# Optimization experiments

Measured on AMD Instinct MI355X. Metric: run time of the kernel, lower is better.

## Reference

```python
import jax, jax.numpy as jnp
import numpy as np
from jax import lax

EPS = 1e-5

def conv2d(x, w, b, pad):
    # x: [N,C,H,W], w: [O,I,kh,kw]
    y = lax.conv_general_dilated(x, w, (1, 1), [(pad, pad), (pad, pad)],
                                 dimension_numbers=('NCHW', 'OIHW', 'NCHW'))
    return y + b[None, :, None, None]

def bn(x, g, b, axes, pshape):
    # training-mode batch norm (biased variance), matching torch BatchNorm2d in train()
    m = jnp.mean(x, axes, keepdims=True)
    v = jnp.var(x, axes, keepdims=True)
    return (x - m) * lax.rsqrt(v + EPS) * g.reshape(pshape) + b.reshape(pshape)

def maxpool2(x):
    return lax.reduce_window(x, -jnp.inf, lax.max, (1, 1, 2, 2), (1, 1, 2, 2), 'VALID')

def setup_inputs() -> dict:
    key = jax.random.key(0)
    ks = jax.random.split(key, 8)
    B, S, C, H, W = 8, 20, 16, 96, 96
    inp = {
        'anchor': jax.random.normal(ks[0], (B, C, H, W), jnp.float32),
        'support': jax.random.normal(ks[1], (B, S, C, H, W), jnp.float32),
        'cw': jax.random.normal(ks[2], (16, 16, 3, 3), jnp.float32) * 0.1,
        'cb': jnp.zeros((16,), jnp.float32),
        'cg': jnp.ones((16,), jnp.float32),
        'cbt': jnp.zeros((16,), jnp.float32),
        'pw': jax.random.normal(ks[3], (16, 32, 1, 1), jnp.float32) * 0.1,
        'pb': jnp.zeros((16,), jnp.float32),
        'pg': jnp.ones((16,), jnp.float32),
        'pbt': jnp.zeros((16,), jnp.float32),
        'jw': jax.random.normal(ks[4], (16, 16, 3, 3), jnp.float32) * 0.1,
        'jb': jnp.zeros((16,), jnp.float32),
        'jg': jnp.ones((16,), jnp.float32),
        'jbt': jnp.zeros((16,), jnp.float32),
        'rw': jax.random.normal(ks[5], (16, 16, 3, 3), jnp.float32) * 0.1,
        'rb': jnp.zeros((16,), jnp.float32),
        'rg': jnp.ones((16,), jnp.float32),
        'rbt': jnp.zeros((16,), jnp.float32),
    }
    return inp

def reference(anchor, support, cw, cb, cg, cbt, pw, pb, pg, pbt,
              jw, jb, jg, jbt, rw, rb, rg, rbt):
    B, S, C, H, W = support.shape
    # reshaper(anchor): conv3x3 -> BN -> ReLU -> maxpool2   (BN stats over B,H,W)
    ax = maxpool2(jax.nn.relu(bn(conv2d(anchor, rw, rb, 1), rg, rbt, (0, 2, 3), (1, -1, 1, 1))))
    # reshaper(support flattened): BN stats pooled over B*S,H,W (matches torch view(-1,...))
    sflat = support.reshape(B * S, C, H, W)
    sr = maxpool2(jax.nn.relu(bn(conv2d(sflat, rw, rb, 1), rg, rbt, (0, 2, 3), (1, -1, 1, 1))))
    sr = sr.reshape(B, S, C, H // 2, W // 2)
    # concentrator(support flattened)
    sx = jax.nn.relu(bn(conv2d(sflat, cw, cb, 1), cg, cbt, (0, 2, 3), (1, -1, 1, 1)))
    sx = sx.reshape(B, S, C, H, W)
    # leave-one-out sum via total-sum trick (O(S) instead of O(S^2))
    loo = sx.sum(axis=1, keepdims=True) - sx              # [B,S,C,H,W]
    cat = jnp.concatenate([support, loo], axis=2)         # [B,S,2C,H,W]
    pe = conv2d(cat.reshape(B * S, 2 * C, H, W), pw, pb, 0).reshape(B, S, C, H, W)
    # torch loop applies perm_equi per-i: BN stats over (B,H,W) for each support index
    pe = jax.nn.relu(bn(pe, pg, pbt, (0, 3, 4), (1, 1, -1, 1, 1)))
    deep = pe.mean(axis=1)                                # [B,C,H,W]
    # projector: conv3x3 -> BN -> softmax over channels -> maxpool2
    proj = maxpool2(jax.nn.softmax(bn(conv2d(deep, jw, jb, 1), jg, jbt, (0, 2, 3), (1, -1, 1, 1)), axis=1))
    anchor_out = ax * proj                                # [B,C,H/2,W/2]
    support_out = sr * proj[:, None]                      # [B,S,C,H/2,W/2]
    return anchor_out, support_out
```

## Files before the change

### kernel.cpp

```cpp
#include <hip/hip_runtime.h>
#include <stdint.h>

#define EPS_BN 1e-5f

typedef __attribute__((ext_vector_type(8))) short short8;
typedef __attribute__((ext_vector_type(4))) float floatx4;

__device__ __forceinline__ unsigned short f2bf(float f) {
    unsigned u = __builtin_bit_cast(unsigned, f);
    u += 0x7fffu + ((u >> 16) & 1u);
    return (unsigned short)(u >> 16);
}
__device__ __forceinline__ float bf2f(unsigned short h) {
    unsigned u = ((unsigned)h) << 16;
    return __builtin_bit_cast(float, u);
}
__device__ __forceinline__ void unpack8(uint4 q, float* v) {
    v[0] = bf2f((unsigned short)q.x); v[1] = bf2f((unsigned short)(q.x >> 16));
    v[2] = bf2f((unsigned short)q.y); v[3] = bf2f((unsigned short)(q.y >> 16));
    v[4] = bf2f((unsigned short)q.z); v[5] = bf2f((unsigned short)(q.z >> 16));
    v[6] = bf2f((unsigned short)q.w); v[7] = bf2f((unsigned short)(q.w >> 16));
}
__device__ __forceinline__ uint4 pack8(const float* v) {
    uint4 q;
    q.x = (unsigned)f2bf(v[0]) | ((unsigned)f2bf(v[1]) << 16);
    q.y = (unsigned)f2bf(v[2]) | ((unsigned)f2bf(v[3]) << 16);
    q.z = (unsigned)f2bf(v[4]) | ((unsigned)f2bf(v[5]) << 16);
    q.w = (unsigned)f2bf(v[6]) | ((unsigned)f2bf(v[7]) << 16);
    return q;
}

__device__ __forceinline__ void async_copy16(const unsigned short* g, unsigned short* l) {
    __builtin_amdgcn_global_load_lds(
        (const __attribute__((address_space(1))) unsigned int*)(const void*)g,
        (__attribute__((address_space(3))) unsigned int*)(void*)l,
        16, 0, 0);
}

__device__ __forceinline__ void bn_coef(const float* st, int n, int c, float invN,
                                        const float* gg, const float* bb,
                                        float* scl, float* shf) {
    const float mean = st[c] * invN;
    const float var = st[n + c] * invN - mean * mean;
    const float sc = gg[c & 15] * rsqrtf(var + EPS_BN);
    scl[c] = sc;
    shf[c] = bb[c & 15] - mean * sc;
}

__global__ __launch_bounds__(256)
void pack_kernel(const float* __restrict__ support, const float* __restrict__ anchor,
                 unsigned short* __restrict__ spad, unsigned short* __restrict__ apad)
{
    const int idx = blockIdx.x * 256 + threadIdx.x;
    if (idx >= 168 * 9604) return;
    const int img = idx / 9604;
    const int rem = idx - img * 9604;
    const int pr = rem / 98, pc = rem - pr * 98;
    const int gh = pr - 1, gw = pc - 1;
    const bool ok = (gh >= 0) & (gh < 96) & (gw >= 0) & (gw < 96);
    const float* src = (img < 160) ? (support + (size_t)img * 147456)
                                   : (anchor + (size_t)(img - 160) * 147456);
    unsigned short* dst = (img < 160) ? (spad + (size_t)img * 9604 * 16)
                                      : (apad + (size_t)(img - 160) * 9604 * 16);
    const int gbase = gh * 96 + gw;
    unsigned pk[8];
    #pragma unroll
    for (int c = 0; c < 8; ++c) {
        const float v0 = ok ? src[(2 * c) * 9216 + gbase] : 0.f;
        const float v1 = ok ? src[(2 * c + 1) * 9216 + gbase] : 0.f;
        pk[c] = (unsigned)f2bf(v0) | ((unsigned)f2bf(v1) << 16);
    }
    const int sw = (pc >> 2) & 1;
    unsigned short* p = dst + (size_t)rem * 16;
    *(uint4*)(p + (sw << 3)) = make_uint4(pk[0], pk[1], pk[2], pk[3]);
    *(uint4*)(p + ((sw ^ 1) << 3)) = make_uint4(pk[4], pk[5], pk[6], pk[7]);
}

__global__ void packw_kernel(const float* __restrict__ rw, const float* __restrict__ cw,
                             const float* __restrict__ jw, unsigned short* __restrict__ frag,
                             float* __restrict__ stats)
{
    const int tid = threadIdx.x;
    if (blockIdx.x == 4) {
        #pragma unroll
        for (int k = 0; k < 3; ++k) stats[k * 256 + tid] = 0.f;
        return;
    }
    const int idx = blockIdx.x * 256 + tid;
    if (idx >= 960) return;
    const int combo = idx >> 6, lane = idx & 63;
    const int cv = combo / 5, j = combo - cv * 5;
    const float* w = (cv == 0) ? rw : (cv == 1) ? cw : jw;
    const int o = lane & 15, g = lane >> 4;
    unsigned short e8[8];
    #pragma unroll
    for (int e = 0; e < 8; ++e) {
        const int k = j * 32 + g * 8 + e;
        unsigned short val = 0;
        if (k < 144) {
            const int t = k >> 4, i = k & 15;
            const int kh = t / 3, kw = t - kh * 3;
            val = f2bf(w[((o * 16 + i) * 3 + kh) * 3 + kw]);
        }
        e8[e] = val;
    }
    *(uint4*)(frag + ((size_t)combo * 64 + lane) * 8) =
        make_uint4((unsigned)e8[0] | ((unsigned)e8[1] << 16), (unsigned)e8[2] | ((unsigned)e8[3] << 16),
                   (unsigned)e8[4] | ((unsigned)e8[5] << 16), (unsigned)e8[6] | ((unsigned)e8[7] << 16));
}

template<bool TWO, bool POOLA>
__global__ __launch_bounds__(256)
void conv3x3_kernel(const unsigned short* __restrict__ in,
                    const unsigned short* __restrict__ fragA, const float* __restrict__ bA,
                    const unsigned short* __restrict__ fragB, const float* __restrict__ bB,
                    unsigned short* __restrict__ outA, unsigned short* __restrict__ outB,
                    float* __restrict__ statsA, float* __restrict__ statsB)
{
    __shared__ __align__(16) unsigned short lds[10 * 98 * 16];
    __shared__ float red[4][4][16];

    const int tid = threadIdx.x;
    const int lane = tid & 63;
    const int wv = tid >> 6;
    const int img = blockIdx.x / 12;
    const int r0b = blockIdx.x - img * 12;

    const unsigned short* gsrc = in + ((size_t)img * 9604 + r0b * 8 * 98) * 16;
    #pragma unroll
    for (int k = 0; k < 8; ++k) {
        const int chunk = k * 256 + tid;
        if (chunk < 1960)
            async_copy16(gsrc + (size_t)chunk * 8, lds + (k * 256 + wv * 64) * 8);
    }

    const int n = lane & 15, g = lane >> 4;
    short8 fA[5], fB[5];
    #pragma unroll
    for (int j = 0; j < 5; ++j) {
        fA[j] = *(const short8*)(fragA + ((size_t)j * 64 + lane) * 8);
        if (TWO) fB[j] = *(const short8*)(fragB + ((size_t)j * 64 + lane) * 8);
    }
    const float4 bA4 = *(const float4*)(bA + 4 * g);
    float4 bB4 = make_float4(0.f, 0.f, 0.f, 0.f);
    if (TWO) bB4 = *(const float4*)(bB + 4 * g);
    const float biasA[4] = {bA4.x, bA4.y, bA4.z, bA4.w};
    const float biasB[4] = {bB4.x, bB4.y, bB4.z, bB4.w};

    __syncthreads();

    float s1A[4] = {0.f, 0.f, 0.f, 0.f}, s2A[4] = {0.f, 0.f, 0.f, 0.f};
    float s1B[4] = {0.f, 0.f, 0.f, 0.f}, s2B[4] = {0.f, 0.f, 0.f, 0.f};

    for (int cg = 0; cg < 6; ++cg) {
        float pA[2][4], pB[2][4];
        #pragma unroll
        for (int tr = 0; tr < 2; ++tr) {
            const int lr = 2 * wv + tr;
            floatx4 aA = {0.f, 0.f, 0.f, 0.f};
            floatx4 aB = {0.f, 0.f, 0.f, 0.f};
            #pragma unroll
            for (int j = 0; j < 5; ++j) {
                const int t = (j < 4) ? (2 * j + (g >> 1)) : 8;
                const int kh = t / 3, kw = t - kh * 3;
                const int ldscol = cg * 16 + n + kw;
                const int half = (g & 1) ^ ((ldscol >> 2) & 1);
                const short8 a = *(const short8*)&lds[((lr + kh) * 98 + ldscol) * 16 + (half << 3)];
                aA = __builtin_amdgcn_mfma_f32_16x16x32_bf16(fA[j], a, aA, 0, 0, 0);
                if (TWO) aB = __builtin_amdgcn_mfma_f32_16x16x32_bf16(fB[j], a, aB, 0, 0, 0);
            }
            #pragma unroll
            for (int r = 0; r < 4; ++r) {
                const float vA = aA[r] + biasA[r];
                pA[tr][r] = vA; s1A[r] += vA; s2A[r] += vA * vA;
                if (TWO) {
                    const float vB = aB[r] + biasB[r];
                    pB[tr][r] = vB; s1B[r] += vB; s2B[r] += vB * vB;
                }
            }
            const int grow = r0b * 8 + lr;
            const size_t pixbase = ((size_t)img * 9216 + grow * 96 + cg * 16 + n) * 16 + 4 * g;
            if (TWO)
                *(uint2*)(outB + pixbase) =
                    make_uint2((unsigned)f2bf(pB[tr][0]) | ((unsigned)f2bf(pB[tr][1]) << 16),
                               (unsigned)f2bf(pB[tr][2]) | ((unsigned)f2bf(pB[tr][3]) << 16));
            if (!POOLA)
                *(uint2*)(outA + pixbase) =
                    make_uint2((unsigned)f2bf(pA[tr][0]) | ((unsigned)f2bf(pA[tr][1]) << 16),
                               (unsigned)f2bf(pA[tr][2]) | ((unsigned)f2bf(pA[tr][3]) << 16));
        }
        if (POOLA) {
            float pm[4];
            #pragma unroll
            for (int r = 0; r < 4; ++r) {
                pm[r] = fmaxf(pA[0][r], pA[1][r]);
                pm[r] = fmaxf(pm[r], __shfl_xor(pm[r], 1));
            }
            if (!(n & 1)) {
                const int orow = r0b * 4 + wv;
                const size_t ob = ((size_t)img * 2304 + orow * 48 + cg * 8 + (n >> 1)) * 16 + 4 * g;
                *(uint2*)(outA + ob) =
                    make_uint2((unsigned)f2bf(pm[0]) | ((unsigned)f2bf(pm[1]) << 16),
                               (unsigned)f2bf(pm[2]) | ((unsigned)f2bf(pm[3]) << 16));
            }
        }
    }

    #pragma unroll
    for (int r = 0; r < 4; ++r) {
        #pragma unroll
        for (int d = 1; d < 16; d <<= 1) {
            s1A[r] += __shfl_xor(s1A[r], d); s2A[r] += __shfl_xor(s2A[r], d);
            if (TWO) { s1B[r] += __shfl_xor(s1B[r], d); s2B[r] += __shfl_xor(s2B[r], d); }
        }
    }
    if (n == 0) {
        #pragma unroll
        for (int r = 0; r < 4; ++r) {
            red[wv][0][g * 4 + r] = s1A[r]; red[wv][1][g * 4 + r] = s2A[r];
            if (TWO) { red[wv][2][g * 4 + r] = s1B[r]; red[wv][3][g * 4 + r] = s2B[r]; }
        }
    }
    __syncthreads();
    if (tid < (TWO ? 64 : 32)) {
        const int st = tid >> 4, oc = tid & 15;
        const float v = red[0][st][oc] + red[1][st][oc] + red[2][st][oc] + red[3][st][oc];
        float* dst = (st < 2) ? statsA : statsB;
        atomicAdd(&dst[(st & 1) * 16 + oc], v);
    }
}

__global__ __launch_bounds__(256)
void sxsum_kernel(const unsigned short* __restrict__ sx, const float* __restrict__ statsSx,
                  const float* __restrict__ cgm, const float* __restrict__ cbt,
                  float* __restrict__ out, unsigned short* __restrict__ deeppad)
{
    __shared__ float scl[16], shf[16];
    __shared__ float part[128][17];
    const int tid = threadIdx.x;
    if (blockIdx.x < 13) {
        const int idx = blockIdx.x * 256 + tid;
        if (idx < 8 * 388) {
            const int img = idx / 388;
            const int h = idx - img * 388;
            int pr, pc;
            if (h < 98)       { pr = 0;           pc = h; }
            else if (h < 196) { pr = 97;          pc = h - 98; }
            else if (h < 292) { pr = h - 196 + 1; pc = 0; }
            else              { pr = h - 292 + 1; pc = 97; }
            unsigned short* p = deeppad + ((size_t)img * 9604 + pr * 98 + pc) * 16;
            *(uint4*)p = make_uint4(0, 0, 0, 0);
            *(uint4*)(p + 8) = make_uint4(0, 0, 0, 0);
        }
    }
    if (tid < 16) bn_coef(statsSx, 16, tid, 1.f / 1474560.f, cgm, cbt, scl, shf);
    const int b = blockIdx.x / 72;
    const int chunk = blockIdx.x - b * 72;
    const int px = tid & 127, sg = tid >> 7;
    const int pix = chunk * 128 + px;
    __syncthreads();
    float acc[16];
    #pragma unroll
    for (int c = 0; c < 16; ++c) acc[c] = 0.f;
    const unsigned short* p = sx + ((size_t)((b * 20) + sg * 10) * 9216 + pix) * 16;
    for (int s = 0; s < 10; ++s) {
        float v[16];
        unpack8(*(const uint4*)p, v);
        unpack8(*(const uint4*)(p + 8), v + 8);
        #pragma unroll
        for (int c = 0; c < 16; ++c) acc[c] += fmaxf(v[c] * scl[c] + shf[c], 0.f);
        p += 9216 * 16;
    }
    if (sg == 1) {
        #pragma unroll
        for (int c = 0; c < 16; ++c) part[px][c] = acc[c];
    }
    __syncthreads();
    if (sg == 0) {
        #pragma unroll
        for (int c = 0; c < 16; ++c) acc[c] += part[px][c];
        float* o = out + ((size_t)b * 9216 + pix) * 16;
        #pragma unroll
        for (int q = 0; q < 4; ++q)
            *(float4*)(o + 4 * q) = make_float4(acc[4 * q], acc[4 * q + 1], acc[4 * q + 2], acc[4 * q + 3]);
    }
}

__global__ __launch_bounds__(256)
void pe_kernel(const unsigned short* __restrict__ spad, unsigned short* __restrict__ sxpe,
               const float* __restrict__ sxsum, const float* __restrict__ statsSx,
               const float* __restrict__ cgm, const float* __restrict__ cbt,
               const float* __restrict__ pw, const float* __restrict__ pb,
               float* __restrict__ statsPe)
{
    __shared__ float sscl[16], sshf[16];
    __shared__ float red[4][2][16];
    const int tid = threadIdx.x;
    if (tid < 16) bn_coef(statsSx, 16, tid, 1.f / 1474560.f, cgm, cbt, sscl, sshf);
    const int lane = tid & 63, wv = tid >> 6;
    const int p = lane & 15, g = lane >> 4;
    const int img = blockIdx.x / 9;
    const int chunk = blockIdx.x - img * 9;
    const int b = img / 20, s = img - b * 20;
    const int c0 = (g & 1) * 8;

    short8 fw;
    {
        const float4 wa = *(const float4*)(pw + p * 32 + g * 8);
        const float4 wb = *(const float4*)(pw + p * 32 + g * 8 + 4);
        fw[0] = (short)f2bf(wa.x); fw[1] = (short)f2bf(wa.y);
        fw[2] = (short)f2bf(wa.z); fw[3] = (short)f2bf(wa.w);
        fw[4] = (short)f2bf(wb.x); fw[5] = (short)f2bf(wb.y);
        fw[6] = (short)f2bf(wb.z); fw[7] = (short)f2bf(wb.w);
    }
    const float4 b4 = *(const float4*)(pb + 4 * g);
    const float bias[4] = {b4.x, b4.y, b4.z, b4.w};
    __syncthreads();
    float scl[8], shf[8];
    #pragma unroll
    for (int e = 0; e < 8; ++e) { scl[e] = sscl[c0 + e]; shf[e] = sshf[c0 + e]; }

    const unsigned short* imgspad = spad + (size_t)img * 9604 * 16;
    unsigned short* imgsx = sxpe + (size_t)img * 9216 * 16;
    const float* bsum = sxsum + (size_t)b * 9216 * 16;

    float s1[4] = {0.f, 0.f, 0.f, 0.f}, s2[4] = {0.f, 0.f, 0.f, 0.f};

    for (int it = 0; it < 16; ++it) {
        const int pix = chunk * 1024 + it * 64 + wv * 16 + p;
        short8 bf;
        if (g < 2) {
            const int row = pix / 96, col = pix - row * 96;
            const int sw = ((col + 1) >> 2) & 1;
            bf = *(const short8*)(imgspad + ((row + 1) * 98 + col + 1) * 16 + (((g ^ sw) & 1) << 3));
        } else {
            float xv[8];
            unpack8(*(const uint4*)(imgsx + (size_t)pix * 16 + c0), xv);
            const float* sm = bsum + (size_t)pix * 16 + c0;
            const float4 sma = *(const float4*)sm;
            const float4 smb = *(const float4*)(sm + 4);
            const float smv[8] = {sma.x, sma.y, sma.z, sma.w, smb.x, smb.y, smb.z, smb.w};
            #pragma unroll
            for (int e = 0; e < 8; ++e) {
                const float loo = smv[e] - fmaxf(xv[e] * scl[e] + shf[e], 0.f);
                bf[e] = (short)f2bf(loo);
            }
        }
        floatx4 acc = {0.f, 0.f, 0.f, 0.f};
        acc = __builtin_amdgcn_mfma_f32_16x16x32_bf16(fw, bf, acc, 0, 0, 0);
        const float v0 = acc[0] + bias[0], v1 = acc[1] + bias[1];
        const float v2 = acc[2] + bias[2], v3 = acc[3] + bias[3];
        s1[0] += v0; s1[1] += v1; s1[2] += v2; s1[3] += v3;
        s2[0] += v0 * v0; s2[1] += v1 * v1; s2[2] += v2 * v2; s2[3] += v3 * v3;
        *(uint2*)(imgsx + (size_t)pix * 16 + 4 * g) =
            make_uint2((unsigned)f2bf(v0) | ((unsigned)f2bf(v1) << 16),
                       (unsigned)f2bf(v2) | ((unsigned)f2bf(v3) << 16));
    }

    #pragma unroll
    for (int r = 0; r < 4; ++r) {
        #pragma unroll
        for (int d = 1; d < 16; d <<= 1) {
            s1[r] += __shfl_xor(s1[r], d);
            s2[r] += __shfl_xor(s2[r], d);
        }
    }
    if (p == 0) {
        #pragma unroll
        for (int r = 0; r < 4; ++r) { red[wv][0][g * 4 + r] = s1[r]; red[wv][1][g * 4 + r] = s2[r]; }
    }
    __syncthreads();
    if (tid < 32) {
        const int st = tid >> 4, c = tid & 15;
        const float v = red[0][st][c] + red[1][st][c] + red[2][st][c] + red[3][st][c];
        atomicAdd(&statsPe[st * 320 + s * 16 + c], v);
    }
}

__global__ __launch_bounds__(256)
void deep_kernel(const unsigned short* __restrict__ pe, const float* __restrict__ statsPe,
                 const float* __restrict__ pg, const float* __restrict__ pbt,
                 unsigned short* __restrict__ deeppad)
{
    __shared__ float scl[320], shf[320];
    __shared__ float part[128][17];
    const int tid = threadIdx.x;
    for (int i = tid; i < 320; i += 256)
        bn_coef(statsPe, 320, i, 1.f / 73728.f, pg, pbt, scl, shf);
    const int b = blockIdx.x / 72;
    const int chunk = blockIdx.x - b * 72;
    const int px = tid & 127, sg = tid >> 7;
    const int pix = chunk * 128 + px;
    __syncthreads();
    float acc[16];
    #pragma unroll
    for (int c = 0; c < 16; ++c) acc[c] = 0.f;
    const unsigned short* p = pe + ((size_t)((b * 20) + sg * 10) * 9216 + pix) * 16;
    for (int s = 0; s < 10; ++s) {
        const int si = sg * 10 + s;
        float v[16];
        unpack8(*(const uint4*)p, v);
        unpack8(*(const uint4*)(p + 8), v + 8);
        #pragma unroll
        for (int c = 0; c < 16; ++c) acc[c] += fmaxf(v[c] * scl[si * 16 + c] + shf[si * 16 + c], 0.f);
        p += 9216 * 16;
    }
    if (sg == 1) {
        #pragma unroll
        for (int c = 0; c < 16; ++c) part[px][c] = acc[c];
    }
    __syncthreads();
    if (sg == 0) {
        #pragma unroll
        for (int c = 0; c < 16; ++c) acc[c] = (acc[c] + part[px][c]) * 0.05f;
        const int row = pix / 96, col = pix - row * 96;
        const int sw = ((col + 1) >> 2) & 1;
        unsigned short* d = deeppad + ((size_t)b * 9604 + (row + 1) * 98 + col + 1) * 16;
        *(uint4*)(d + (sw << 3)) = pack8(acc);
        *(uint4*)(d + ((sw ^ 1) << 3)) = pack8(acc + 8);
    }
}

__global__ __launch_bounds__(256)
void proj_kernel(const unsigned short* __restrict__ pj, const float* __restrict__ statsJ,
                 const float* __restrict__ jg, const float* __restrict__ jbt,
                 float* __restrict__ proj)
{
    __shared__ float scl[16], shf[16];
    const int tid = threadIdx.x;
    if (tid < 16) bn_coef(statsJ, 16, tid, 1.f / 73728.f, jg, jbt, scl, shf);
    const int b = blockIdx.x / 9;
    const int opix = (blockIdx.x - b * 9) * 256 + tid;
    __syncthreads();
    const int oi = opix / 48, oj = opix - oi * 48;
    float mx[16];
    #pragma unroll
    for (int c = 0; c < 16; ++c) mx[c] = 0.f;
    #pragma unroll
    for (int dy = 0; dy < 2; ++dy) {
        const unsigned short* q = pj + ((size_t)b * 9216 + (2 * oi + dy) * 96 + 2 * oj) * 16;
        #pragma unroll
        for (int dx = 0; dx < 2; ++dx) {
            float v[16]; float mval = -1e30f;
            unpack8(*(const uint4*)(q + dx * 16), v);
            unpack8(*(const uint4*)(q + dx * 16 + 8), v + 8);
            #pragma unroll
            for (int c = 0; c < 16; ++c) { v[c] = v[c] * scl[c] + shf[c]; mval = fmaxf(mval, v[c]); }
            float ssum = 0.f;
            #pragma unroll
            for (int c = 0; c < 16; ++c) { v[c] = __expf(v[c] - mval); ssum += v[c]; }
            const float inv = 1.f / ssum;
            #pragma unroll
            for (int c = 0; c < 16; ++c) mx[c] = fmaxf(mx[c], v[c] * inv);
        }
    }
    float* o = proj + ((size_t)b * 2304 + opix) * 16;
    #pragma unroll
    for (int q2 = 0; q2 < 4; ++q2)
        *(float4*)(o + 4 * q2) = make_float4(mx[4 * q2], mx[4 * q2 + 1], mx[4 * q2 + 2], mx[4 * q2 + 3]);
}

__global__ __launch_bounds__(256)
void out_anchor_kernel(const unsigned short* __restrict__ axp, const float* __restrict__ statsAx,
                       const float* __restrict__ rg, const float* __restrict__ rbt,
                       const float* __restrict__ proj, float* __restrict__ out)
{
    __shared__ float scl[16], shf[16];
    const int tid = threadIdx.x;
    if (tid < 16) bn_coef(statsAx, 16, tid, 1.f / 73728.f, rg, rbt, scl, shf);
    const int b = blockIdx.x / 9;
    const int opix = (blockIdx.x - b * 9) * 256 + tid;
    __syncthreads();
    const unsigned short* p = axp + ((size_t)b * 2304 + opix) * 16;
    float v[16];
    unpack8(*(const uint4*)p, v);
    unpack8(*(const uint4*)(p + 8), v + 8);
    const float* pr = proj + ((size_t)b * 2304 + opix) * 16;
    #pragma unroll
    for (int c = 0; c < 16; ++c)
        out[((size_t)b * 16 + c) * 2304 + opix] = fmaxf(v[c] * scl[c] + shf[c], 0.f) * pr[c];
}

__global__ __launch_bounds__(256)
void out_support_kernel(const unsigned short* __restrict__ srp, const float* __restrict__ statsSr,
                        const float* __restrict__ rg, const float* __restrict__ rbt,
                        const float* __restrict__ proj, float* __restrict__ out)
{
    __shared__ float scl[16], shf[16];
    const int tid = threadIdx.x;
    if (tid < 16) bn_coef(statsSr, 16, tid, 1.f / 1474560.f, rg, rbt, scl, shf);
    const int bs = blockIdx.x / 9;
    const int opix = (blockIdx.x - bs * 9) * 256 + tid;
    const int b = bs / 20;
    __syncthreads();
    const unsigned short* p = srp + ((size_t)bs * 2304 + opix) * 16;
    float v[16];
    unpack8(*(const uint4*)p, v);
    unpack8(*(const uint4*)(p + 8), v + 8);
    const float* pr = proj + ((size_t)b * 2304 + opix) * 16;
    #pragma unroll
    for (int c = 0; c < 16; ++c)
        out[((size_t)bs * 16 + c) * 2304 + opix] = fmaxf(v[c] * scl[c] + shf[c], 0.f) * pr[c];
}

extern "C" void kernel_launch(void* const* d_in, const int* in_sizes, int n_in,
                              void* d_out, int out_size, void* d_ws, size_t ws_size,
                              hipStream_t stream)
{
    const float* anchor  = (const float*)d_in[0];
    const float* support = (const float*)d_in[1];
    const float* cw  = (const float*)d_in[2];
    const float* cb  = (const float*)d_in[3];
    const float* cgm = (const float*)d_in[4];
    const float* cbt = (const float*)d_in[5];
    const float* pw  = (const float*)d_in[6];
    const float* pb  = (const float*)d_in[7];
    const float* pg  = (const float*)d_in[8];
    const float* pbt = (const float*)d_in[9];
    const float* jw  = (const float*)d_in[10];
    const float* jb  = (const float*)d_in[11];
    const float* jg  = (const float*)d_in[12];
    const float* jbt = (const float*)d_in[13];
    const float* rw  = (const float*)d_in[14];
    const float* rb  = (const float*)d_in[15];
    const float* rg  = (const float*)d_in[16];
    const float* rbt = (const float*)d_in[17];
    float* out = (float*)d_out;

    char* ws = (char*)d_ws;
    unsigned short* spad    = (unsigned short*)ws;
    unsigned short* pre_j   = (unsigned short*)(ws + 2458624);
    float*          proj    = (float*)(ws + 4817920);
    unsigned short* apad    = (unsigned short*)(ws + 49172480);
    unsigned short* deeppad = apad;
    unsigned short* sxpe    = (unsigned short*)(ws + 51631104);
    unsigned short* srp     = (unsigned short*)(ws + 98817024);
    unsigned short* axp     = (unsigned short*)(ws + 110613504);
    float*          sxsum   = (float*)(ws + 111203328);
    unsigned short* frag    = (unsigned short*)(ws + 115921920);
    float*          stats   = (float*)(ws + 115937280);

    unsigned short* fragR = frag;
    unsigned short* fragC = frag + 5 * 64 * 8;
    unsigned short* fragJ = frag + 10 * 64 * 8;
    float* statsAx = stats,      *statsSr = stats + 32, *statsSx = stats + 64;
    float* statsPe = stats + 96, *statsJ  = stats + 736;

    pack_kernel<<<6303, 256, 0, stream>>>(support, anchor, spad, apad);
    packw_kernel<<<5, 256, 0, stream>>>(rw, cw, jw, frag, stats);

    conv3x3_kernel<true, true><<<1920, 256, 0, stream>>>(
        spad, fragR, rb, fragC, cb, srp, sxpe, statsSr, statsSx);
    conv3x3_kernel<false, true><<<96, 256, 0, stream>>>(
        apad, fragR, rb, nullptr, nullptr, axp, nullptr, statsAx, nullptr);
    sxsum_kernel<<<576, 256, 0, stream>>>(sxpe, statsSx, cgm, cbt, sxsum, deeppad);
    pe_kernel<<<1440, 256, 0, stream>>>(spad, sxpe, sxsum, statsSx, cgm, cbt, pw, pb, statsPe);
    deep_kernel<<<576, 256, 0, stream>>>(sxpe, statsPe, pg, pbt, deeppad);
    conv3x3_kernel<false, false><<<96, 256, 0, stream>>>(
        deeppad, fragJ, jb, nullptr, nullptr, pre_j, nullptr, statsJ, nullptr);
    proj_kernel<<<72, 256, 0, stream>>>(pre_j, statsJ, jg, jbt, proj);
    out_anchor_kernel<<<72, 256, 0, stream>>>(axp, statsAx, rg, rbt, proj, out);
    out_support_kernel<<<1440, 256, 0, stream>>>(srp, statsSr, rg, rbt, proj, out + 294912);
}
```

Baseline: 153.1 us.

## Merge small kernels into combined launches and split S-reduction across four groups

Folds weight packing and stats zeroing into the input pack kernel, merges the support and anchor conv launches into one grid, and merges the two output kernels into one. This cuts launch count and lets the small anchor work run alongside the support work instead of as separate, under-occupied launches. The sxsum and deep reductions now use four support groups of 5 over 64-pixel chunks, giving twice as many blocks for more parallelism. The conv kernel now takes a runtime 'two' flag instead of a template parameter, which may add divergence or register pressure.

Result: faster. 144.8 us (-5.5%).

```diff
diff --git a/kernel.cpp b/kernel.cpp
--- a/kernel.cpp
+++ b/kernel.cpp
@@ -49,9 +49,43 @@
 
 __global__ __launch_bounds__(256)
 void pack_kernel(const float* __restrict__ support, const float* __restrict__ anchor,
-                 unsigned short* __restrict__ spad, unsigned short* __restrict__ apad)
-{
-    const int idx = blockIdx.x * 256 + threadIdx.x;
+                 unsigned short* __restrict__ spad, unsigned short* __restrict__ apad,
+                 const float* __restrict__ rw, const float* __restrict__ cw,
+                 const float* __restrict__ jw, unsigned short* __restrict__ frag,
+                 float* __restrict__ stats)
+{
+    const int tid = threadIdx.x;
+    if (blockIdx.x >= 6303) {
+        const int bx = blockIdx.x - 6303;
+        if (bx == 4) {
+            #pragma unroll
+            for (int k = 0; k < 3; ++k) stats[k * 256 + tid] = 0.f;
+            return;
+        }
+        const int idx = bx * 256 + tid;
+        if (idx >= 960) return;
+        const int combo = idx >> 6, lane = idx & 63;
+        const int cv = combo / 5, j = combo - cv * 5;
+        const float* w = (cv == 0) ? rw : (cv == 1) ? cw : jw;
+        const int o = lane & 15, g = lane >> 4;
+        unsigned short e8[8];
+        #pragma unroll
+        for (int e = 0; e < 8; ++e) {
+            const int k = j * 32 + g * 8 + e;
+            unsigned short val = 0;
+            if (k < 144) {
+                const int t = k >> 4, i = k & 15;
+                const int kh = t / 3, kw = t - kh * 3;
+                val = f2bf(w[((o * 16 + i) * 3 + kh) * 3 + kw]);
+            }
+            e8[e] = val;
+        }
+        *(uint4*)(frag + ((size_t)combo * 64 + lane) * 8) =
+            make_uint4((unsigned)e8[0] | ((unsigned)e8[1] << 16), (unsigned)e8[2] | ((unsigned)e8[3] << 16),
+                       (unsigned)e8[4] | ((unsigned)e8[5] << 16), (unsigned)e8[6] | ((unsigned)e8[7] << 16));
+        return;
+    }
+    const int idx = blockIdx.x * 256 + tid;
     if (idx >= 168 * 9604) return;
     const int img = idx / 9604;
     const int rem = idx - img * 9604;
@@ -76,57 +110,21 @@
     *(uint4*)(p + ((sw ^ 1) << 3)) = make_uint4(pk[4], pk[5], pk[6], pk[7]);
 }
 
-__global__ void packw_kernel(const float* __restrict__ rw, const float* __restrict__ cw,
-                             const float* __restrict__ jw, unsigned short* __restrict__ frag,
-                             float* __restrict__ stats)
-{
-    const int tid = threadIdx.x;
-    if (blockIdx.x == 4) {
-        #pragma unroll
-        for (int k = 0; k < 3; ++k) stats[k * 256 + tid] = 0.f;
-        return;
-    }
-    const int idx = blockIdx.x * 256 + tid;
-    if (idx >= 960) return;
-    const int combo = idx >> 6, lane = idx & 63;
-    const int cv = combo / 5, j = combo - cv * 5;
-    const float* w = (cv == 0) ? rw : (cv == 1) ? cw : jw;
-    const int o = lane & 15, g = lane >> 4;
-    unsigned short e8[8];
-    #pragma unroll
-    for (int e = 0; e < 8; ++e) {
-        const int k = j * 32 + g * 8 + e;
-        unsigned short val = 0;
-        if (k < 144) {
-            const int t = k >> 4, i = k & 15;
-            const int kh = t / 3, kw = t - kh * 3;
-            val = f2bf(w[((o * 16 + i) * 3 + kh) * 3 + kw]);
-        }
-        e8[e] = val;
-    }
-    *(uint4*)(frag + ((size_t)combo * 64 + lane) * 8) =
-        make_uint4((unsigned)e8[0] | ((unsigned)e8[1] << 16), (unsigned)e8[2] | ((unsigned)e8[3] << 16),
-                   (unsigned)e8[4] | ((unsigned)e8[5] << 16), (unsigned)e8[6] | ((unsigned)e8[7] << 16));
-}
-
-template<bool TWO, bool POOLA>
-__global__ __launch_bounds__(256)
-void conv3x3_kernel(const unsigned short* __restrict__ in,
-                    const unsigned short* __restrict__ fragA, const float* __restrict__ bA,
-                    const unsigned short* __restrict__ fragB, const float* __restrict__ bB,
-                    unsigned short* __restrict__ outA, unsigned short* __restrict__ outB,
-                    float* __restrict__ statsA, float* __restrict__ statsB)
-{
-    __shared__ __align__(16) unsigned short lds[10 * 98 * 16];
-    __shared__ float red[4][4][16];
-
+template<bool POOLA>
+__device__ __forceinline__ void conv_tile(
+    unsigned short* lds, float* red,
+    const unsigned short* __restrict__ imgin,
+    const unsigned short* __restrict__ fragA, const float* __restrict__ bA,
+    const unsigned short* __restrict__ fragB, const float* __restrict__ bB,
+    unsigned short* __restrict__ outAimg, unsigned short* __restrict__ outBimg,
+    float* __restrict__ statsA, float* __restrict__ statsB,
+    const int r0b, const bool two)
+{
     const int tid = threadIdx.x;
     const int lane = tid & 63;
     const int wv = tid >> 6;
-    const int img = blockIdx.x / 12;
-    const int r0b = blockIdx.x - img * 12;
-
-    const unsigned short* gsrc = in + ((size_t)img * 9604 + r0b * 8 * 98) * 16;
+
+    const unsigned short* gsrc = imgin + (size_t)(r0b * 8 * 98) * 16;
     #pragma unroll
     for (int k = 0; k < 8; ++k) {
         const int chunk = k * 256 + tid;
@@ -139,11 +137,11 @@
     #pragma unroll
     for (int j = 0; j < 5; ++j) {
         fA[j] = *(const short8*)(fragA + ((size_t)j * 64 + lane) * 8);
-        if (TWO) fB[j] = *(const short8*)(fragB + ((size_t)j * 64 + lane) * 8);
+        if (two) fB[j] = *(const short8*)(fragB + ((size_t)j * 64 + lane) * 8);
     }
     const float4 bA4 = *(const float4*)(bA + 4 * g);
     float4 bB4 = make_float4(0.f, 0.f, 0.f, 0.f);
-    if (TWO) bB4 = *(const float4*)(bB + 4 * g);
+    if (two) bB4 = *(const float4*)(bB + 4 * g);
     const float biasA[4] = {bA4.x, bA4.y, bA4.z, bA4.w};
     const float biasB[4] = {bB4.x, bB4.y, bB4.z, bB4.w};
 
@@ -167,25 +165,25 @@
                 const int half = (g & 1) ^ ((ldscol >> 2) & 1);
                 const short8 a = *(const short8*)&lds[((lr + kh) * 98 + ldscol) * 16 + (half << 3)];
                 aA = __builtin_amdgcn_mfma_f32_16x16x32_bf16(fA[j], a, aA, 0, 0, 0);
-                if (TWO) aB = __builtin_amdgcn_mfma_f32_16x16x32_bf16(fB[j], a, aB, 0, 0, 0);
+                if (two) aB = __builtin_amdgcn_mfma_f32_16x16x32_bf16(fB[j], a, aB, 0, 0, 0);
             }
             #pragma unroll
             for (int r = 0; r < 4; ++r) {
                 const float vA = aA[r] + biasA[r];
                 pA[tr][r] = vA; s1A[r] += vA; s2A[r] += vA * vA;
-                if (TWO) {
+                if (two) {
                     const float vB = aB[r] + biasB[r];
                     pB[tr][r] = vB; s1B[r] += vB; s2B[r] += vB * vB;
                 }
             }
             const int grow = r0b * 8 + lr;
-            const size_t pixbase = ((size_t)img * 9216 + grow * 96 + cg * 16 + n) * 16 + 4 * g;
-            if (TWO)
-                *(uint2*)(outB + pixbase) =
+            const size_t pixbase = ((size_t)(grow * 96 + cg * 16 + n)) * 16 + 4 * g;
+            if (two)
+                *(uint2*)(outBimg + pixbase) =
                     make_uint2((unsigned)f2bf(pB[tr][0]) | ((unsigned)f2bf(pB[tr][1]) << 16),
                                (unsigned)f2bf(pB[tr][2]) | ((unsigned)f2bf(pB[tr][3]) << 16));
             if (!POOLA)
-                *(uint2*)(outA + pixbase) =
+                *(uint2*)(outAimg + pixbase) =
                     make_uint2((unsigned)f2bf(pA[tr][0]) | ((unsigned)f2bf(pA[tr][1]) << 16),
                                (unsigned)f2bf(pA[tr][2]) | ((unsigned)f2bf(pA[tr][3]) << 16));
         }
@@ -198,8 +196,8 @@
             }
             if (!(n & 1)) {
                 const int orow = r0b * 4 + wv;
-                const size_t ob = ((size_t)img * 2304 + orow * 48 + cg * 8 + (n >> 1)) * 16 + 4 * g;
-                *(uint2*)(outA + ob) =
+                const size_t ob = ((size_t)(orow * 48 + cg * 8 + (n >> 1))) * 16 + 4 * g;
+                *(uint2*)(outAimg + ob) =
                     make_uint2((unsigned)f2bf(pm[0]) | ((unsigned)f2bf(pm[1]) << 16),
                                (unsigned)f2bf(pm[2]) | ((unsigned)f2bf(pm[3]) << 16));
             }
@@ -211,23 +209,63 @@
         #pragma unroll
         for (int d = 1; d < 16; d <<= 1) {
             s1A[r] += __shfl_xor(s1A[r], d); s2A[r] += __shfl_xor(s2A[r], d);
-            if (TWO) { s1B[r] += __shfl_xor(s1B[r], d); s2B[r] += __shfl_xor(s2B[r], d); }
+            if (two) { s1B[r] += __shfl_xor(s1B[r], d); s2B[r] += __shfl_xor(s2B[r], d); }
         }
     }
     if (n == 0) {
         #pragma unroll
         for (int r = 0; r < 4; ++r) {
-            red[wv][0][g * 4 + r] = s1A[r]; red[wv][1][g * 4 + r] = s2A[r];
-            if (TWO) { red[wv][2][g * 4 + r] = s1B[r]; red[wv][3][g * 4 + r] = s2B[r]; }
-        }
-    }
-    __syncthreads();
-    if (tid < (TWO ? 64 : 32)) {
+            red[(wv * 4 + 0) * 16 + g * 4 + r] = s1A[r];
+            red[(wv * 4 + 1) * 16 + g * 4 + r] = s2A[r];
+            if (two) {
+                red[(wv * 4 + 2) * 16 + g * 4 + r] = s1B[r];
+                red[(wv * 4 + 3) * 16 + g * 4 + r] = s2B[r];
+            }
+        }
+    }
+    __syncthreads();
+    if (tid < (two ? 64 : 32)) {
         const int st = tid >> 4, oc = tid & 15;
-        const float v = red[0][st][oc] + red[1][st][oc] + red[2][st][oc] + red[3][st][oc];
+        const float v = red[(0 * 4 + st) * 16 + oc] + red[(1 * 4 + st) * 16 + oc] +
+                        red[(2 * 4 + st) * 16 + oc] + red[(3 * 4 + st) * 16 + oc];
         float* dst = (st < 2) ? statsA : statsB;
         atomicAdd(&dst[(st & 1) * 16 + oc], v);
     }
+}
+
+__global__ __launch_bounds__(256)
+void conv_main_kernel(const unsigned short* __restrict__ spad, const unsigned short* __restrict__ apad,
+                      const unsigned short* __restrict__ fragR, const float* __restrict__ rb,
+                      const unsigned short* __restrict__ fragC, const float* __restrict__ cb,
+                      unsigned short* __restrict__ srp, unsigned short* __restrict__ sxpe,
+                      unsigned short* __restrict__ axp,
+                      float* __restrict__ statsSr, float* __restrict__ statsSx,
+                      float* __restrict__ statsAx)
+{
+    __shared__ __align__(16) unsigned short lds[10 * 98 * 16];
+    __shared__ float red[4 * 4 * 16];
+    const bool two = blockIdx.x < 1920;
+    const int bid = two ? blockIdx.x : blockIdx.x - 1920;
+    const int img = bid / 12;
+    const int r0b = bid - img * 12;
+    const unsigned short* in = (two ? spad : apad) + (size_t)img * 9604 * 16;
+    unsigned short* outA = (two ? srp : axp) + (size_t)img * 2304 * 16;
+    unsigned short* outB = sxpe + (size_t)img * 9216 * 16;
+    conv_tile<true>(lds, red, in, fragR, rb, fragC, cb, outA, outB,
+                    two ? statsSr : statsAx, statsSx, r0b, two);
+}
+
+__global__ __launch_bounds__(256)
+void conv_j_kernel(const unsigned short* __restrict__ deeppad,
+                   const unsigned short* __restrict__ fragJ, const float* __restrict__ jb,
+                   unsigned short* __restrict__ pre_j, float* __restrict__ statsJ)
+{
+    __shared__ __align__(16) unsigned short lds[10 * 98 * 16];
+    __shared__ float red[4 * 4 * 16];
+    const int img = blockIdx.x / 12;
+    const int r0b = blockIdx.x - img * 12;
+    conv_tile<false>(lds, red, deeppad + (size_t)img * 9604 * 16, fragJ, jb, nullptr, nullptr,
+                     pre_j + (size_t)img * 9216 * 16, nullptr, statsJ, nullptr, r0b, false);
 }
 
 __global__ __launch_bounds__(256)
@@ -236,7 +274,7 @@
                   float* __restrict__ out, unsigned short* __restrict__ deeppad)
 {
     __shared__ float scl[16], shf[16];
-    __shared__ float part[128][17];
+    __shared__ float part[3][64][17];
     const int tid = threadIdx.x;
     if (blockIdx.x < 13) {
         const int idx = blockIdx.x * 256 + tid;
@@ -254,16 +292,17 @@
         }
     }
     if (tid < 16) bn_coef(statsSx, 16, tid, 1.f / 1474560.f, cgm, cbt, scl, shf);
-    const int b = blockIdx.x / 72;
-    const int chunk = blockIdx.x - b * 72;
-    const int px = tid & 127, sg = tid >> 7;
-    const int pix = chunk * 128 + px;
+    const int b = blockIdx.x / 144;
+    const int chunk = blockIdx.x - b * 144;
+    const int px = tid & 63, sg = tid >> 6;
+    const int pix = chunk * 64 + px;
     __syncthreads();
     float acc[16];
     #pragma unroll
     for (int c = 0; c < 16; ++c) acc[c] = 0.f;
-    const unsigned short* p = sx + ((size_t)((b * 20) + sg * 10) * 9216 + pix) * 16;
-    for (int s = 0; s < 10; ++s) {
+    const unsigned short* p = sx + ((size_t)(b * 20 + sg * 5) * 9216 + pix) * 16;
+    #pragma unroll
+    for (int s = 0; s < 5; ++s) {
         float v[16];
         unpack8(*(const uint4*)p, v);
         unpack8(*(const uint4*)(p + 8), v + 8);
@@ -271,14 +310,14 @@
         for (int c = 0; c < 16; ++c) acc[c] += fmaxf(v[c] * scl[c] + shf[c], 0.f);
         p += 9216 * 16;
     }
-    if (sg == 1) {
-        #pragma unroll
-        for (int c = 0; c < 16; ++c) part[px][c] = acc[c];
+    if (sg > 0) {
+        #pragma unroll
+        for (int c = 0; c < 16; ++c) part[sg - 1][px][c] = acc[c];
     }
     __syncthreads();
     if (sg == 0) {
         #pragma unroll
-        for (int c = 0; c < 16; ++c) acc[c] += part[px][c];
+        for (int c = 0; c < 16; ++c) acc[c] += part[0][px][c] + part[1][px][c] + part[2][px][c];
         float* o = out + ((size_t)b * 9216 + pix) * 16;
         #pragma unroll
         for (int q = 0; q < 4; ++q)
@@ -383,21 +422,22 @@
                  unsigned short* __restrict__ deeppad)
 {
     __shared__ float scl[320], shf[320];
-    __shared__ float part[128][17];
+    __shared__ float part[3][64][17];
     const int tid = threadIdx.x;
     for (int i = tid; i < 320; i += 256)
         bn_coef(statsPe, 320, i, 1.f / 73728.f, pg, pbt, scl, shf);
-    const int b = blockIdx.x / 72;
-    const int chunk = blockIdx.x - b * 72;
-    const int px = tid & 127, sg = tid >> 7;
-    const int pix = chunk * 128 + px;
+    const int b = blockIdx.x / 144;
+    const int chunk = blockIdx.x - b * 144;
+    const int px = tid & 63, sg = tid >> 6;
+    const int pix = chunk * 64 + px;
     __syncthreads();
     float acc[16];
     #pragma unroll
     for (int c = 0; c < 16; ++c) acc[c] = 0.f;
-    const unsigned short* p = pe + ((size_t)((b * 20) + sg * 10) * 9216 + pix) * 16;
-    for (int s = 0; s < 10; ++s) {
-        const int si = sg * 10 + s;
+    const unsigned short* p = pe + ((size_t)(b * 20 + sg * 5) * 9216 + pix) * 16;
+    #pragma unroll
+    for (int s = 0; s < 5; ++s) {
+        const int si = sg * 5 + s;
         float v[16];
         unpack8(*(const uint4*)p, v);
         unpack8(*(const uint4*)(p + 8), v + 8);
@@ -405,14 +445,15 @@
         for (int c = 0; c < 16; ++c) acc[c] += fmaxf(v[c] * scl[si * 16 + c] + shf[si * 16 + c], 0.f);
         p += 9216 * 16;
     }
-    if (sg == 1) {
-        #pragma unroll
-        for (int c = 0; c < 16; ++c) part[px][c] = acc[c];
+    if (sg > 0) {
+        #pragma unroll
+        for (int c = 0; c < 16; ++c) part[sg - 1][px][c] = acc[c];
     }
     __syncthreads();
     if (sg == 0) {
         #pragma unroll
-        for (int c = 0; c < 16; ++c) acc[c] = (acc[c] + part[px][c]) * 0.05f;
+        for (int c = 0; c < 16; ++c)
+            acc[c] = (acc[c] + part[0][px][c] + part[1][px][c] + part[2][px][c]) * 0.05f;
         const int row = pix / 96, col = pix - row * 96;
         const int sw = ((col + 1) >> 2) & 1;
         unsigned short* d = deeppad + ((size_t)b * 9604 + (row + 1) * 98 + col + 1) * 16;
@@ -461,46 +502,33 @@
 }
 
 __global__ __launch_bounds__(256)
-void out_anchor_kernel(const unsigned short* __restrict__ axp, const float* __restrict__ statsAx,
-                       const float* __restrict__ rg, const float* __restrict__ rbt,
-                       const float* __restrict__ proj, float* __restrict__ out)
+void out_kernel(const unsigned short* __restrict__ srp, const unsigned short* __restrict__ axp,
+                const float* __restrict__ statsSr, const float* __restrict__ statsAx,
+                const float* __restrict__ rg, const float* __restrict__ rbt,
+                const float* __restrict__ proj, float* __restrict__ outS,
+                float* __restrict__ outA)
 {
     __shared__ float scl[16], shf[16];
     const int tid = threadIdx.x;
-    if (tid < 16) bn_coef(statsAx, 16, tid, 1.f / 73728.f, rg, rbt, scl, shf);
-    const int b = blockIdx.x / 9;
-    const int opix = (blockIdx.x - b * 9) * 256 + tid;
-    __syncthreads();
-    const unsigned short* p = axp + ((size_t)b * 2304 + opix) * 16;
+    const bool sup = blockIdx.x < 1440;
+    if (tid < 16) {
+        if (sup) bn_coef(statsSr, 16, tid, 1.f / 1474560.f, rg, rbt, scl, shf);
+        else     bn_coef(statsAx, 16, tid, 1.f / 73728.f, rg, rbt, scl, shf);
+    }
+    const int bid = sup ? blockIdx.x : blockIdx.x - 1440;
+    const int bs = bid / 9;
+    const int opix = (bid - bs * 9) * 256 + tid;
+    const int b = sup ? bs / 20 : bs;
+    __syncthreads();
+    const unsigned short* p = (sup ? srp : axp) + ((size_t)bs * 2304 + opix) * 16;
     float v[16];
     unpack8(*(const uint4*)p, v);
     unpack8(*(const uint4*)(p + 8), v + 8);
     const float* pr = proj + ((size_t)b * 2304 + opix) * 16;
+    float* o = sup ? outS : outA;
     #pragma unroll
     for (int c = 0; c < 16; ++c)
-        out[((size_t)b * 16 + c) * 2304 + opix] = fmaxf(v[c] * scl[c] + shf[c], 0.f) * pr[c];
-}
-
-__global__ __launch_bounds__(256)
-void out_support_kernel(const unsigned short* __restrict__ srp, const float* __restrict__ statsSr,
-                        const float* __restrict__ rg, const float* __restrict__ rbt,
-                        const float* __restrict__ proj, float* __restrict__ out)
-{
-    __shared__ float scl[16], shf[16];
-    const int tid = threadIdx.x;
-    if (tid < 16) bn_coef(statsSr, 16, tid, 1.f / 1474560.f, rg, rbt, scl, shf);
-    const int bs = blockIdx.x / 9;
-    const int opix = (blockIdx.x - bs * 9) * 256 + tid;
-    const int b = bs / 20;
-    __syncthreads();
-    const unsigned short* p = srp + ((size_t)bs * 2304 + opix) * 16;
-    float v[16];
-    unpack8(*(const uint4*)p, v);
-    unpack8(*(const uint4*)(p + 8), v + 8);
-    const float* pr = proj + ((size_t)b * 2304 + opix) * 16;
-    #pragma unroll
-    for (int c = 0; c < 16; ++c)
-        out[((size_t)bs * 16 + c) * 2304 + opix] = fmaxf(v[c] * scl[c] + shf[c], 0.f) * pr[c];
+        o[((size_t)bs * 16 + c) * 2304 + opix] = fmaxf(v[c] * scl[c] + shf[c], 0.f) * pr[c];
 }
 
 extern "C" void kernel_launch(void* const* d_in, const int* in_sizes, int n_in,
@@ -546,19 +574,14 @@
     float* statsAx = stats,      *statsSr = stats + 32, *statsSx = stats + 64;
     float* statsPe = stats + 96, *statsJ  = stats + 736;
 
-    pack_kernel<<<6303, 256, 0, stream>>>(support, anchor, spad, apad);
-    packw_kernel<<<5, 256, 0, stream>>>(rw, cw, jw, frag, stats);
-
-    conv3x3_kernel<true, true><<<1920, 256, 0, stream>>>(
-        spad, fragR, rb, fragC, cb, srp, sxpe, statsSr, statsSx);
-    conv3x3_kernel<false, true><<<96, 256, 0, stream>>>(
-        apad, fragR, rb, nullptr, nullptr, axp, nullptr, statsAx, nullptr);
-    sxsum_kernel<<<576, 256, 0, stream>>>(sxpe, statsSx, cgm, cbt, sxsum, deeppad);
+    pack_kernel<<<6308, 256, 0, stream>>>(support, anchor, spad, apad, rw, cw, jw, frag, stats);
+    conv_main_kernel<<<2016, 256, 0, stream>>>(spad, apad, fragR, rb, fragC, cb,
+                                               srp, sxpe, axp, statsSr, statsSx, statsAx);
+    sxsum_kernel<<<1152, 256, 0, stream>>>(sxpe, statsSx, cgm, cbt, sxsum, deeppad);
     pe_kernel<<<1440, 256, 0, stream>>>(spad, sxpe, sxsum, statsSx, cgm, cbt, pw, pb, statsPe);
-    deep_kernel<<<576, 256, 0, stream>>>(sxpe, statsPe, pg, pbt, deeppad);
-    conv3x3_kernel<false, false><<<96, 256, 0, stream>>>(
-        deeppad, fragJ, jb, nullptr, nullptr, pre_j, nullptr, statsJ, nullptr);
+    deep_kernel<<<1152, 256, 0, stream>>>(sxpe, statsPe, pg, pbt, deeppad);
+    conv_j_kernel<<<96, 256, 0, stream>>>(deeppad, fragJ, jb, pre_j, statsJ);
     proj_kernel<<<72, 256, 0, stream>>>(pre_j, statsJ, jg, jbt, proj);
-    out_anchor_kernel<<<72, 256, 0, stream>>>(axp, statsAx, rg, rbt, proj, out);
-    out_support_kernel<<<1440, 256, 0, stream>>>(srp, statsSr, rg, rbt, proj, out + 294912);
-}
+    out_kernel<<<1512, 256, 0, stream>>>(srp, axp, statsSr, statsAx, rg, rbt, proj,
+                                         out + 294912, out);
+}
```
